# Optimization experiments

Hardware: AMD Instinct MI355X
Metric: run time of the kernel (lower is better)

Reference implementation:

```python
import jax, jax.numpy as jnp
import numpy as np

R_MAX = 5.0
AVG_NEIGH = 16.0
NUM_RADIAL = 8
F = 64            # channels per irrep (num_features)
S = 10            # num_species
LDIM = 16         # (max_ell+1)^2 for max_ell=3
L_SLICES = [(0, 1), (1, 4), (4, 9), (9, 16)]  # lm ranges for l=0..3
N_NODES = 10000
N_EDGES = 160000
HID_R = 64        # radial MLP hidden
HID_READ = 32     # readout MLP hidden


def sph_harm(v):
    # real spherical-harmonic polynomials up to l=3 (component convention fixed by this reference)
    x, y, z = v[:, 0], v[:, 1], v[:, 2]
    r2 = x * x + y * y + z * z
    return jnp.stack([
        jnp.ones_like(x),
        x, y, z,
        x * y, y * z, 3.0 * z * z - r2, x * z, x * x - y * y,
        y * (3.0 * x * x - y * y), x * y * z, y * (5.0 * z * z - r2),
        z * (5.0 * z * z - 3.0 * r2), x * (5.0 * z * z - r2),
        z * (x * x - y * y), x * (x * x - 3.0 * y * y),
    ], axis=-1)  # [E,16]


def radial_embedding(r):
    # Bessel basis with polynomial envelope (RadialEmbeddingBlock)
    u = r / R_MAX
    k = jnp.arange(1, NUM_RADIAL + 1, dtype=r.dtype)
    env = jnp.where(u < 1.0, (1.0 - u) ** 2 * (1.0 + 2.0 * u), 0.0)
    return jnp.sin(jnp.pi * k[None, :] * u[:, None]) / (u[:, None] + 1e-6) * env[:, None]


def species_linear(feats, W):
    # species-indexed e3nn Linear: per-l channel mixing. feats [N,F,16], W [N,4,F,F]
    outs = []
    for l, (a, b) in enumerate(L_SLICES):
        outs.append(jnp.einsum('nfm,nfg->ngm', feats[:, :, a:b], W[:, l]))
    return jnp.concatenate(outs, axis=-1)


def interaction(feats, Y, Remb, w1, w2, senders, receivers, n_nodes):
    # InteractionBlock: radial MLP -> tensor-product messages -> scatter-sum
    E = Y.shape[0]
    R = (jax.nn.silu(Remb @ w1) @ w2).reshape(E, F, 4, 2)  # per-l, per-path radial weights
    fs = feats[senders]            # [E,F,16] gather (irregular access)
    s0 = fs[:, :, 0:1]             # sender scalar channel
    parts = []
    for l, (a, b) in enumerate(L_SLICES):
        # path A: 0e (x) l -> l ;  path B: l (x) 0e -> l
        m_l = R[:, :, l, 0:1] * s0 * Y[:, None, a:b] + R[:, :, l, 1:2] * fs[:, :, a:b]
        parts.append(m_l)
    m = jnp.concatenate(parts, axis=-1)  # [E,F,16]
    agg = jax.ops.segment_sum(m, receivers, num_segments=n_nodes)
    return agg / jnp.sqrt(jnp.asarray(AVG_NEIGH, m.dtype))


def setup_inputs() -> dict:
    key = jax.random.key(0)
    ks = jax.random.split(key, 16)
    inp = {
        'vectors': jax.random.normal(ks[0], (N_EDGES, 3), jnp.float32) * 1.5,
        'node_specie': jax.random.randint(ks[1], (N_NODES,), 0, S, jnp.int32),
        'senders': jax.random.randint(ks[2], (N_EDGES,), 0, N_NODES, jnp.int32),
        'receivers': jax.random.randint(ks[3], (N_EDGES,), 0, N_NODES, jnp.int32),
        'w_embed': jax.random.normal(ks[4], (S, F), jnp.float32),
        'w_r1': jax.random.normal(ks[5], (2, NUM_RADIAL, HID_R), jnp.float32) / np.sqrt(NUM_RADIAL),
        'w_r2': jax.random.normal(ks[6], (2, HID_R, F * 4 * 2), jnp.float32) / np.sqrt(HID_R),
        'w_skip': jax.random.normal(ks[7], (2, S, 4, F, F), jnp.float32) / np.sqrt(F),
        'w_poly': jax.random.normal(ks[8], (2, 3, S, F), jnp.float32) * 0.1,
        'w_read0': jax.random.normal(ks[9], (F, 1), jnp.float32) / np.sqrt(F),
        'w_mlp1': jax.random.normal(ks[10], (F, HID_READ), jnp.float32) / np.sqrt(F),
        'w_mlp2': jax.random.normal(ks[11], (HID_READ, 1), jnp.float32) / np.sqrt(HID_READ),
    }
    return inp


def reference(vectors, node_specie, senders, receivers,
              w_embed, w_r1, w_r2, w_skip, w_poly,
              w_read0, w_mlp1, w_mlp2):
    N = node_specie.shape[0]
    senders = senders.astype(jnp.int32)
    receivers = receivers.astype(jnp.int32)
    r = jnp.sqrt(jnp.sum(vectors ** 2, axis=-1) + 1e-12)
    Y = sph_harm(vectors / r[:, None])
    Remb = radial_embedding(r)
    # node embedding -> scalar (l=0) channel only
    feats = jnp.zeros((N, F, LDIM), vectors.dtype).at[:, :, 0].set(w_embed[node_specie])
    outs = []
    for i in range(2):
        Wn = w_skip[i][node_specie]  # [N,4,F,F] species-indexed weights
        if i == 0:
            agg = interaction(feats, Y, Remb, w_r1[i], w_r2[i], senders, receivers, N)
            h = species_linear(agg, Wn)   # skip_tp_first
            sc = None
        else:
            sc = species_linear(feats, Wn)  # skip connection
            h = interaction(feats, Y, Remb, w_r1[i], w_r2[i], senders, receivers, N)
        # EquivariantProductBasisBlock (correlation=3): degree-3 invariant polynomial gate
        c = w_poly[i][:, node_specie]       # [3,N,F]
        s = h[:, :, 0]
        scale = c[0] + c[1] * s + c[2] * s * s
        feats = h * scale[:, :, None]
        if sc is not None:
            feats = feats + sc
        if i == 0:
            outs.append(feats[:, :, 0] @ w_read0)                       # LinearReadoutBlock
        else:
            outs.append(jax.nn.silu(feats[:, :, 0] @ w_mlp1) @ w_mlp2)  # NonLinearReadoutBlock
    return jnp.stack(outs, axis=1)  # [N, num_interactions, 1]
```

## Files before the change

### kernel.cpp

```cpp
#include <hip/hip_runtime.h>
#include <math.h>

#define F 64
#define LDIM 16
#define NRAD 8
#define HID_R 64
#define HID_READ 32
#define NSPEC 10

typedef __attribute__((ext_vector_type(8))) short short8v;
typedef __attribute__((ext_vector_type(4))) float f32x4;

__device__ __forceinline__ int l_of_m(int m) {
    return (m == 0) ? 0 : (m < 4) ? 1 : (m < 9) ? 2 : 3;
}
__device__ __forceinline__ float silu(float x) { return x / (1.0f + __expf(-x)); }
__device__ __forceinline__ unsigned short bf16bits(float x) {
    unsigned int u = __float_as_uint(x);
    u += 0x7fffu + ((u >> 16) & 1u);
    return (unsigned short)(u >> 16);
}
__device__ __forceinline__ float bf16tof(unsigned short b) {
    return __uint_as_float(((unsigned int)b) << 16);
}
__device__ __forceinline__ float lanebcast(float v, int l) {
    return __uint_as_float(__builtin_amdgcn_readlane(__float_as_uint(v), l));
}

__device__ __forceinline__ void geo_core(const float* __restrict__ vectors, int e,
                                         float* Ye_out, float* remb_out) {
    float vx = vectors[e * 3 + 0];
    float vy = vectors[e * 3 + 1];
    float vz = vectors[e * 3 + 2];
    float r = sqrtf(vx * vx + vy * vy + vz * vz + 1e-12f);
    float x = vx / r, y = vy / r, z = vz / r;
    float r2 = x * x + y * y + z * z;
    Ye_out[0]  = 1.0f;  Ye_out[1] = x;  Ye_out[2] = y;  Ye_out[3] = z;
    Ye_out[4]  = x * y; Ye_out[5] = y * z; Ye_out[6] = 3.0f * z * z - r2; Ye_out[7] = x * z;
    Ye_out[8]  = x * x - y * y;
    Ye_out[9]  = y * (3.0f * x * x - y * y);
    Ye_out[10] = x * y * z;
    Ye_out[11] = y * (5.0f * z * z - r2);
    Ye_out[12] = z * (5.0f * z * z - 3.0f * r2);
    Ye_out[13] = x * (5.0f * z * z - r2);
    Ye_out[14] = z * (x * x - y * y);
    Ye_out[15] = x * (x * x - 3.0f * y * y);
    float u = r / 5.0f;
    float env = (u < 1.0f) ? (1.0f - u) * (1.0f - u) * (1.0f + 2.0f * u) : 0.0f;
    float inv = env / (u + 1e-6f);
    const float PI = 3.14159265358979323846f;
#pragma unroll
    for (int k = 1; k <= NRAD; k++) remb_out[k - 1] = sinf(PI * (float)k * u) * inv;
}

__device__ __forceinline__ void hid_write(const float* remb, const float* w1,
                                          unsigned short* __restrict__ Hb, int e) {
    float h[HID_R];
#pragma unroll
    for (int j = 0; j < HID_R; j++) {
        float a = 0.0f;
#pragma unroll
        for (int k = 0; k < NRAD; k++) a += remb[k] * w1[k * HID_R + j];
        h[j] = silu(a);
    }
    unsigned int* dst = (unsigned int*)(Hb + (size_t)e * HID_R);
#pragma unroll
    for (int w = 0; w < 32; w++) {
        unsigned int lo = bf16bits(h[2 * w]);
        unsigned int hi = bf16bits(h[2 * w + 1]);
        dst[w] = lo | (hi << 16);
    }
}

__global__ void k1_kernel(const float* __restrict__ vectors,
                          const float* __restrict__ w_r1,
                          const float* __restrict__ w_r2,
                          const int* __restrict__ receivers,
                          float* __restrict__ Y,
                          unsigned short* __restrict__ Hb,
                          int* __restrict__ cnt,
                          unsigned short* __restrict__ w2f,
                          int E, int ngeo) {
    const int bid = blockIdx.x;
    if (bid >= ngeo) {
        const int layer = bid - ngeo;
        const float* src = w_r2 + (size_t)layer * HID_R * 512;
        unsigned short* dst = w2f + (size_t)layer * 32768;
        for (int idx = threadIdx.x; idx < 32768; idx += 256) {
            int j    = idx & 7;
            int lane = (idx >> 3) & 63;
            int ks   = (idx >> 9) & 1;
            int ct   = idx >> 10;
            int k    = ks * 32 + (lane >> 4) * 8 + j;
            int col  = ct * 16 + (lane & 15);
            dst[idx] = bf16bits(src[k * 512 + col]);
        }
        return;
    }
    const int e = bid * 256 + threadIdx.x;
    if (e >= E) return;
    atomicAdd(&cnt[receivers[e]], 1);
    float ye[16], remb[NRAD];
    geo_core(vectors, e, ye, remb);
    float4* Yd = (float4*)(Y + (size_t)e * 16);
    Yd[0] = make_float4(ye[0], ye[1], ye[2], ye[3]);
    Yd[1] = make_float4(ye[4], ye[5], ye[6], ye[7]);
    Yd[2] = make_float4(ye[8], ye[9], ye[10], ye[11]);
    Yd[3] = make_float4(ye[12], ye[13], ye[14], ye[15]);
    hid_write(remb, w_r1, Hb, e);
}

__global__ void geo_kernel(const float* __restrict__ vectors,
                           float* __restrict__ Y, float* __restrict__ Remb, int E) {
    int e = blockIdx.x * 256 + threadIdx.x;
    if (e >= E) return;
    float ye[16], remb[NRAD];
    geo_core(vectors, e, ye, remb);
#pragma unroll
    for (int m = 0; m < 16; m++) Y[(size_t)e * 16 + m] = ye[m];
#pragma unroll
    for (int k = 0; k < NRAD; k++) Remb[(size_t)e * NRAD + k] = remb[k];
}

__global__ void scan_kernel(const int* __restrict__ cnt, int* __restrict__ offs, int N) {
    __shared__ int buf[256];
    __shared__ int carry;
    int t = threadIdx.x;
    if (t == 0) carry = 0;
    __syncthreads();
    for (int base = 0; base < N; base += 256) {
        int v = (base + t < N) ? cnt[base + t] : 0;
        buf[t] = v;
        __syncthreads();
#pragma unroll
        for (int off = 1; off < 256; off <<= 1) {
            int x = (t >= off) ? buf[t - off] : 0;
            __syncthreads();
            buf[t] += x;
            __syncthreads();
        }
        if (base + t < N) offs[base + t] = carry + buf[t] - v;
        __syncthreads();
        if (t == 0) carry += buf[255];
        __syncthreads();
    }
    if (t == 0) offs[N] = carry;
}

__global__ void scatter_kernel(const int* __restrict__ receivers,
                               const int* __restrict__ senders,
                               const int* __restrict__ offs, int* __restrict__ cur,
                               int* __restrict__ eidx, int* __restrict__ snd_csr,
                               int* __restrict__ rcv_csr, int E) {
    int e = blockIdx.x * 256 + threadIdx.x;
    if (e >= E) return;
    int r = receivers[e];
    int pos = atomicAdd(&cur[r], 1);
    int t = offs[r] + pos;
    eidx[t] = e;
    snd_csr[t] = senders[e];
    rcv_csr[t] = r;
}

__global__ void init_feats_kernel(const float* __restrict__ w_embed,
                                  const int* __restrict__ specie,
                                  float* __restrict__ feats_t, int N) {
    int n = blockIdx.x;
    int sp = specie[n];
    for (int i = threadIdx.x; i < F * LDIM; i += 256) {
        int m = i >> 6;
        int f = i & 63;
        feats_t[(size_t)n * (F * LDIM) + i] = (m == 0) ? w_embed[sp * F + f] : 0.0f;
    }
}

template <bool L0>
__global__ __launch_bounds__(256, 4)
void fused_edge_kernel(const unsigned short* __restrict__ Hb,
                       const unsigned short* __restrict__ w2fl,
                       const float* __restrict__ Y,
                       const unsigned short* __restrict__ featsB,
                       const float* __restrict__ w_embed,
                       const int* __restrict__ specie,
                       const int* __restrict__ offs,
                       const int* __restrict__ eidx,
                       const int* __restrict__ snd_csr,
                       const int* __restrict__ rcv_csr,
                       float* __restrict__ agg, int N) {
    __shared__ float R_lds[16 * 532];
    __shared__ float ysL[16][16];
    __shared__ int   ssL[16];
    __shared__ int   rsL[16];
    const int tid = threadIdx.x;
    const int wave = tid >> 6, lane = tid & 63;
    const int lo = lane & 15, hi = lane >> 4;
    const int n0 = blockIdx.x * 2;
    const int segS = offs[n0], segE = offs[n0 + 2];
    const int mbase = wave * 4;

    int cur = -1;
    float acc[4] = {0.f, 0.f, 0.f, 0.f};

    for (int base = segS; base < segE; base += 16) {
        const int bend = (base + 16 < segE) ? base + 16 : segE;
        const int tcnt = bend - base;
        {
            const int t = tid >> 4, m = tid & 15;
            const int pos = base + t;
            const int cp = (pos < segE) ? pos : (segE - 1);
            ysL[t][m] = Y[(size_t)eidx[cp] * 16 + m];
            if (tid < 16) {
                const int p2 = base + tid;
                const int c2 = (p2 < segE) ? p2 : (segE - 1);
                const int s = snd_csr[c2];
                ssL[tid] = L0 ? specie[s] : s;
                rsL[tid] = rcv_csr[c2];
            }
        }
        {
            const int pos = base + lo;
            const int cp = (pos < segE) ? pos : (segE - 1);
            const int eid = eidx[cp];
            const unsigned short* hrow = Hb + (size_t)eid * 64;
            const short8v a0 = *(const short8v*)(hrow + hi * 8);
            const short8v a1 = *(const short8v*)(hrow + 32 + hi * 8);
            f32x4 c16[8];
#pragma unroll
            for (int i = 0; i < 8; i++) c16[i] = (f32x4)(0.f);
#pragma unroll
            for (int tt = 0; tt < 8; tt++) {
                const int ct = wave * 8 + tt;
                const short8v b0 = *(const short8v*)(w2fl + ct * 1024 + lane * 8);
                const short8v b1 = *(const short8v*)(w2fl + ct * 1024 + 512 + lane * 8);
                c16[tt] = __builtin_amdgcn_mfma_f32_16x16x32_bf16(a0, b0, c16[tt], 0, 0, 0);
                c16[tt] = __builtin_amdgcn_mfma_f32_16x16x32_bf16(a1, b1, c16[tt], 0, 0, 0);
            }
            const int lc = lo & 7;
#pragma unroll
            for (int tt = 0; tt < 8; tt++) {
                const int ct = wave * 8 + tt;
                const int f = ct * 2 + (lo >> 3);
#pragma unroll
                for (int r = 0; r < 4; r++) {
                    const int el = hi * 4 + r;
                    R_lds[el * 532 + lc * 66 + f] = c16[tt][r];
                }
            }
        }
        __syncthreads();
        {
            float ps0, pf[4] = {0.f, 0.f, 0.f, 0.f};
            if (L0) {
                ps0 = w_embed[ssL[0] * 64 + lane];
            } else {
                const unsigned short* f_ = featsB + (size_t)ssL[0] * 1024;
                ps0 = bf16tof(f_[lane]);
#pragma unroll
                for (int j = 0; j < 4; j++) pf[j] = bf16tof(f_[(mbase + j) * 64 + lane]);
            }
            for (int k = 0; k < tcnt; k++) {
                float ns0 = 0.f, nf[4] = {0.f, 0.f, 0.f, 0.f};
                const int kn = (k + 1 < tcnt) ? k + 1 : k;
                if (L0) {
                    ns0 = w_embed[ssL[kn] * 64 + lane];
                } else {
                    const unsigned short* f_ = featsB + (size_t)ssL[kn] * 1024;
                    ns0 = bf16tof(f_[lane]);
#pragma unroll
                    for (int j = 0; j < 4; j++) nf[j] = bf16tof(f_[(mbase + j) * 64 + lane]);
                }
                const int node = rsL[k];
                if (node != cur) {
                    if (cur >= 0) {
#pragma unroll
                        for (int j = 0; j < 4; j++)
                            agg[(size_t)cur * 1024 + (mbase + j) * 64 + lane] = acc[j] * 0.25f;
                    }
#pragma unroll
                    for (int j = 0; j < 4; j++) acc[j] = 0.f;
                    cur = node;
                }
                const float* Rt = R_lds + k * 532;
#pragma unroll
                for (int j = 0; j < 4; j++) {
                    const int m = mbase + j;
                    const int l = l_of_m(m);
                    const float r0 = Rt[(2 * l) * 66 + lane];
                    const float r1 = Rt[(2 * l + 1) * 66 + lane];
                    const float ym = ysL[k][m];
                    const float fsm = L0 ? ((m == 0) ? ps0 : 0.f) : pf[j];
                    acc[j] += r0 * ps0 * ym + r1 * fsm;
                }
                ps0 = ns0;
                if (!L0) {
#pragma unroll
                    for (int j = 0; j < 4; j++) pf[j] = nf[j];
                }
            }
        }
        __syncthreads();
    }
    if (cur >= 0) {
#pragma unroll
        for (int j = 0; j < 4; j++)
            agg[(size_t)cur * 1024 + (mbase + j) * 64 + lane] = acc[j] * 0.25f;
    }
#pragma unroll
    for (int d = 0; d < 2; d++) {
        const int nn = n0 + d;
        if (nn < N && offs[nn] == offs[nn + 1]) {
#pragma unroll
            for (int j = 0; j < 4; j++)
                agg[(size_t)nn * 1024 + (mbase + j) * 64 + lane] = 0.f;
        }
    }
}

__global__ void k2_kernel(const float* __restrict__ agg,
                          const int* __restrict__ specie,
                          const float* __restrict__ w_skip0,
                          const float* __restrict__ w_poly0,
                          const float* __restrict__ w_read0,
                          unsigned short* __restrict__ featsB,
                          float* __restrict__ featsF,
                          int useBF16,
                          float* __restrict__ out, int N,
                          const float* __restrict__ vectors,
                          const float* __restrict__ w1L1,
                          unsigned short* __restrict__ Hb, int E) {
    if (blockIdx.x >= N) {
        const int e = (blockIdx.x - N) * 256 + threadIdx.x;
        if (e >= E) return;
        float ye[16], remb[NRAD];
        geo_core(vectors, e, ye, remb);
        hid_write(remb, w1L1, Hb, e);
        return;
    }
    const int n = blockIdx.x;
    const int g = threadIdx.x & 63;
    const int mb = threadIdx.x >> 6;
    const int sp = specie[n];
    const float* W = w_skip0 + (size_t)sp * 4 * F * F;

    float areg[4];
#pragma unroll
    for (int j = 0; j < 4; j++) areg[j] = agg[(size_t)n * 1024 + (mb * 4 + j) * 64 + g];

    float h[4] = {0.f, 0.f, 0.f, 0.f};
    if (mb == 0) {
        const float* W0 = W;
        const float* W1 = W + 4096;
#pragma unroll
        for (int f = 0; f < 64; f++) {
            const float w0 = W0[f * 64 + g];
            const float w1 = W1[f * 64 + g];
            h[0] += lanebcast(areg[0], f) * w0;
            h[1] += lanebcast(areg[1], f) * w1;
            h[2] += lanebcast(areg[2], f) * w1;
            h[3] += lanebcast(areg[3], f) * w1;
        }
    } else if (mb == 1) {
        const float* W2 = W + 8192;
#pragma unroll
        for (int f = 0; f < 64; f++) {
            const float w2 = W2[f * 64 + g];
            h[0] += lanebcast(areg[0], f) * w2;
            h[1] += lanebcast(areg[1], f) * w2;
            h[2] += lanebcast(areg[2], f) * w2;
            h[3] += lanebcast(areg[3], f) * w2;
        }
    } else if (mb == 2) {
        const float* W2 = W + 8192;
        const float* W3 = W + 12288;
#pragma unroll
        for (int f = 0; f < 64; f++) {
            const float w2 = W2[f * 64 + g];
            const float w3 = W3[f * 64 + g];
            h[0] += lanebcast(areg[0], f) * w2;
            h[1] += lanebcast(areg[1], f) * w3;
            h[2] += lanebcast(areg[2], f) * w3;
            h[3] += lanebcast(areg[3], f) * w3;
        }
    } else {
        const float* W3 = W + 12288;
#pragma unroll
        for (int f = 0; f < 64; f++) {
            const float w3 = W3[f * 64 + g];
            h[0] += lanebcast(areg[0], f) * w3;
            h[1] += lanebcast(areg[1], f) * w3;
            h[2] += lanebcast(areg[2], f) * w3;
            h[3] += lanebcast(areg[3], f) * w3;
        }
    }

    __shared__ float h0L[64];
    if (mb == 0) h0L[g] = h[0];
    __syncthreads();
    const float s = h0L[g];
    const float c0 = w_poly0[(0 * NSPEC + sp) * F + g];
    const float c1 = w_poly0[(1 * NSPEC + sp) * F + g];
    const float c2 = w_poly0[(2 * NSPEC + sp) * F + g];
    const float scale = c0 + c1 * s + c2 * s * s;
    float f0val = 0.0f;
#pragma unroll
    for (int j = 0; j < 4; j++) {
        const int m = mb * 4 + j;
        const float fv = h[j] * scale;
        const size_t idx = (size_t)n * 1024 + m * 64 + g;
        if (useBF16) featsB[idx] = bf16bits(fv);
        else         featsF[idx] = fv;
        if (m == 0) f0val = fv;
    }
    if (mb == 0) {
        float v = f0val * w_read0[g];
#pragma unroll
        for (int off = 32; off > 0; off >>= 1) v += __shfl_down(v, off);
        if (g == 0) out[(size_t)n * 2 + 0] = v;
    }
}

__global__ void node1_kernel(const float* __restrict__ agg,
                             const unsigned short* __restrict__ featsB,
                             const int* __restrict__ specie,
                             const float* __restrict__ w_skip1,
                             const float* __restrict__ w_poly1,
                             const float* __restrict__ w_mlp1,
                             const float* __restrict__ w_mlp2,
                             float* __restrict__ out, int N) {
    const int wave = threadIdx.x >> 6;
    const int lane = threadIdx.x & 63;
    const int n = blockIdx.x * 4 + wave;
    const int sp = specie[n];
    const float* W0 = w_skip1 + (size_t)sp * 4 * F * F;
    const float fv = bf16tof(featsB[(size_t)n * 1024 + lane]);
    float sc0 = 0.0f;
#pragma unroll
    for (int f = 0; f < F; f++) {
        sc0 += lanebcast(fv, f) * W0[f * F + lane];
    }
    const float h0 = agg[(size_t)n * 1024 + lane];
    const float c0 = w_poly1[(0 * NSPEC + sp) * F + lane];
    const float c1 = w_poly1[(1 * NSPEC + sp) * F + lane];
    const float c2 = w_poly1[(2 * NSPEC + sp) * F + lane];
    const float scale = c0 + c1 * h0 + c2 * h0 * h0;
    const float f2 = h0 * scale + sc0;
    float acc = 0.0f;
#pragma unroll
    for (int gg = 0; gg < F; gg++) {
        const float fg = lanebcast(f2, gg);
        if (lane < HID_READ) acc += fg * w_mlp1[gg * HID_READ + lane];
    }
    float o = 0.0f;
    if (lane < HID_READ) o = silu(acc) * w_mlp2[lane];
#pragma unroll
    for (int off = 32; off > 0; off >>= 1) o += __shfl_down(o, off);
    if (lane == 0) out[(size_t)n * 2 + 1] = o;
}

__global__ void node1f_kernel(const float* __restrict__ agg,
                              const float* __restrict__ feats,
                              const int* __restrict__ specie,
                              const float* __restrict__ w_skip1,
                              const float* __restrict__ w_poly1,
                              const float* __restrict__ w_mlp1,
                              const float* __restrict__ w_mlp2,
                              float* __restrict__ out, int N) {
    const int wave = threadIdx.x >> 6;
    const int lane = threadIdx.x & 63;
    const int n = blockIdx.x * 4 + wave;
    const int sp = specie[n];
    const float* W0 = w_skip1 + (size_t)sp * 4 * F * F;
    const float fv = feats[(size_t)n * 1024 + lane];
    float sc0 = 0.0f;
#pragma unroll 8
    for (int f = 0; f < F; f++) {
        const float ff = __shfl(fv, f);
        sc0 += ff * W0[f * F + lane];
    }
    const float h0 = agg[(size_t)n * 1024 + lane];
    const float c0 = w_poly1[(0 * NSPEC + sp) * F + lane];
    const float c1 = w_poly1[(1 * NSPEC + sp) * F + lane];
    const float c2 = w_poly1[(2 * NSPEC + sp) * F + lane];
    const float scale = c0 + c1 * h0 + c2 * h0 * h0;
    const float f2 = h0 * scale + sc0;
    float acc = 0.0f;
#pragma unroll 8
    for (int gg = 0; gg < F; gg++) {
        const float fg = __shfl(f2, gg);
        if (lane < HID_READ) acc += fg * w_mlp1[gg * HID_READ + lane];
    }
    float o = 0.0f;
    if (lane < HID_READ) o = silu(acc) * w_mlp2[lane];
#pragma unroll
    for (int off = 32; off > 0; off >>= 1) o += __shfl_down(o, off);
    if (lane == 0) out[(size_t)n * 2 + 1] = o;
}

__global__ void edge_kernel(const float* __restrict__ Y, const float* __restrict__ Remb,
                            const float* __restrict__ feats_t,
                            const int* __restrict__ senders, const int* __restrict__ receivers,
                            const float* __restrict__ w1, const float* __restrict__ w2,
                            float* __restrict__ agg_t, int E) {
    const int wave = threadIdx.x >> 6;
    const int lane = threadIdx.x & 63;
    const int e = blockIdx.x * 4 + wave;
    __shared__ float hbuf[4][64];
    const float* remb = Remb + (size_t)e * NRAD;
    float acc = 0.0f;
#pragma unroll
    for (int k = 0; k < NRAD; k++) acc += remb[k] * w1[k * F + lane];
    hbuf[wave][lane] = silu(acc);
    __syncthreads();
    float r8[8] = {0.f, 0.f, 0.f, 0.f, 0.f, 0.f, 0.f, 0.f};
    const float* w2base = w2 + lane * 8;
#pragma unroll 8
    for (int j = 0; j < HID_R; j++) {
        float hj = hbuf[wave][j];
        const float4 a = *(const float4*)(w2base + j * 512);
        const float4 b = *(const float4*)(w2base + j * 512 + 4);
        r8[0] += hj * a.x; r8[1] += hj * a.y; r8[2] += hj * a.z; r8[3] += hj * a.w;
        r8[4] += hj * b.x; r8[5] += hj * b.y; r8[6] += hj * b.z; r8[7] += hj * b.w;
    }
    const int snd = senders[e];
    const int rcv = receivers[e];
    const float* fsrc = feats_t + (size_t)snd * (F * LDIM);
    float* adst = agg_t + (size_t)rcv * (F * LDIM);
    const float s0 = fsrc[lane];
    const float* Ye = Y + (size_t)e * 16;
#pragma unroll
    for (int m = 0; m < LDIM; m++) {
        const int l = l_of_m(m);
        const float ym = Ye[m];
        const float fsm = fsrc[m * F + lane];
        const float val = r8[l * 2 + 0] * s0 * ym + r8[l * 2 + 1] * fsm;
        atomicAdd(adst + m * F + lane, val * 0.25f);
    }
}

static inline size_t alignup(size_t x) { return (x + 255) & ~(size_t)255; }

extern "C" void kernel_launch(void* const* d_in, const int* in_sizes, int n_in,
                              void* d_out, int out_size, void* d_ws, size_t ws_size,
                              hipStream_t stream) {
    const float* vectors   = (const float*)d_in[0];
    const int*   specie    = (const int*)d_in[1];
    const int*   senders   = (const int*)d_in[2];
    const int*   receivers = (const int*)d_in[3];
    const float* w_embed   = (const float*)d_in[4];
    const float* w_r1      = (const float*)d_in[5];
    const float* w_r2      = (const float*)d_in[6];
    const float* w_skip    = (const float*)d_in[7];
    const float* w_poly    = (const float*)d_in[8];
    const float* w_read0   = (const float*)d_in[9];
    const float* w_mlp1    = (const float*)d_in[10];
    const float* w_mlp2    = (const float*)d_in[11];
    float* out = (float*)d_out;

    const int E = in_sizes[0] / 3;
    const int N = in_sizes[1];
    const int ngeo = (E + 255) / 256;

    char* base = (char*)d_ws;
    size_t off = 0;
    float* Y      = (float*)(base + off); off += alignup((size_t)E * 16 * sizeof(float));
    unsigned short* featsB = (unsigned short*)(base + off); off += alignup((size_t)N * F * LDIM * sizeof(unsigned short));
    float* agg    = (float*)(base + off); off += alignup((size_t)N * F * LDIM * sizeof(float));
    unsigned short* Hb = (unsigned short*)(base + off); off += alignup((size_t)E * 64 * sizeof(unsigned short));
    int* cnt      = (int*)(base + off);   off += alignup((size_t)N * sizeof(int));
    int* cur      = (int*)(base + off);   off += alignup((size_t)N * sizeof(int));
    int* offs     = (int*)(base + off);   off += alignup((size_t)(N + 1) * sizeof(int));
    int* eidx     = (int*)(base + off);   off += alignup((size_t)E * sizeof(int));
    int* snd_csr  = (int*)(base + off);   off += alignup((size_t)E * sizeof(int));
    int* rcv_csr  = (int*)(base + off);   off += alignup((size_t)E * sizeof(int));
    unsigned short* w2f = (unsigned short*)(base + off); off += alignup((size_t)2 * 32768 * sizeof(unsigned short));
    const size_t need = off;

    const size_t aggBytes = (size_t)N * F * LDIM * sizeof(float);

    if (ws_size >= need) {
        hipMemsetAsync(cnt, 0, (size_t)N * sizeof(int), stream);
        hipMemsetAsync(cur, 0, (size_t)N * sizeof(int), stream);
        k1_kernel<<<ngeo + 2, 256, 0, stream>>>(vectors, w_r1, w_r2, receivers,
                                                Y, Hb, cnt, w2f, E, ngeo);
        scan_kernel<<<1, 256, 0, stream>>>(cnt, offs, N);
        scatter_kernel<<<ngeo, 256, 0, stream>>>(receivers, senders, offs, cur,
                                                 eidx, snd_csr, rcv_csr, E);
        fused_edge_kernel<true><<<N / 2, 256, 0, stream>>>(
            Hb, w2f, Y, nullptr, w_embed, specie, offs, eidx, snd_csr, rcv_csr, agg, N);
        k2_kernel<<<N + ngeo, 256, 0, stream>>>(agg, specie,
                                                w_skip + (size_t)0 * NSPEC * 4 * F * F,
                                                w_poly + (size_t)0 * 3 * NSPEC * F,
                                                w_read0, featsB, nullptr, 1, out, N,
                                                vectors, w_r1 + NRAD * HID_R, Hb, E);
        fused_edge_kernel<false><<<N / 2, 256, 0, stream>>>(
            Hb, w2f + 32768, Y, featsB, w_embed, specie, offs, eidx, snd_csr, rcv_csr, agg, N);
        node1_kernel<<<N / 4, 256, 0, stream>>>(agg, featsB, specie,
                                                w_skip + (size_t)1 * NSPEC * 4 * F * F,
                                                w_poly + (size_t)1 * 3 * NSPEC * F,
                                                w_mlp1, w_mlp2, out, N);
    } else {
        size_t fo = 0;
        float* Yf    = (float*)(base + fo); fo += alignup((size_t)E * 16 * sizeof(float));
        float* Remb  = (float*)(base + fo); fo += alignup((size_t)E * NRAD * sizeof(float));
        float* featsF= (float*)(base + fo); fo += alignup((size_t)N * F * LDIM * sizeof(float));
        float* aggF  = (float*)(base + fo);

        geo_kernel<<<ngeo, 256, 0, stream>>>(vectors, Yf, Remb, E);
        init_feats_kernel<<<N, 256, 0, stream>>>(w_embed, specie, featsF, N);
        hipMemsetAsync(aggF, 0, aggBytes, stream);
        edge_kernel<<<E / 4, 256, 0, stream>>>(Yf, Remb, featsF, senders, receivers,
                                               w_r1, w_r2, aggF, E);
        k2_kernel<<<N, 256, 0, stream>>>(aggF, specie,
                                         w_skip + (size_t)0 * NSPEC * 4 * F * F,
                                         w_poly + (size_t)0 * 3 * NSPEC * F,
                                         w_read0, nullptr, featsF, 0, out, N,
                                         vectors, w_r1 + NRAD * HID_R, nullptr, 0);
        hipMemsetAsync(aggF, 0, aggBytes, stream);
        edge_kernel<<<E / 4, 256, 0, stream>>>(Yf, Remb, featsF, senders, receivers,
                                               w_r1 + NRAD * HID_R, w_r2 + HID_R * 512,
                                               aggF, E);
        node1f_kernel<<<N / 4, 256, 0, stream>>>(aggF, featsF, specie,
                                                 w_skip + (size_t)1 * NSPEC * 4 * F * F,
                                                 w_poly + (size_t)1 * 3 * NSPEC * F,
                                                 w_mlp1, w_mlp2, out, N);
    }
}
```

Measured before the change: 387.4 us.

## Assign one wave per receiver node with channel-major bf16 features and wider scan

The edge kernel now handles four receiver nodes per block, and each wave owns one node and accumulates all 16 lm components in registers. This replaces the old split where each wave held four components and tracked node changes through a receiver CSR array, so the rcv_csr array and its writes go away. The bf16 feature buffer is transposed so each lane reads its 16 components with two 16-byte vector loads, and the prefix scan uses 1024 threads. In exchange, three of the four waves sit idle while each 16-edge tile's per-node work runs, and register pressure rises with 16 accumulators.

```diff
diff --git a/kernel.cpp b/kernel.cpp
--- a/kernel.cpp
+++ b/kernel.cpp
@@ -123,17 +123,17 @@
 }
 
 __global__ void scan_kernel(const int* __restrict__ cnt, int* __restrict__ offs, int N) {
-    __shared__ int buf[256];
+    __shared__ int buf[1024];
     __shared__ int carry;
     int t = threadIdx.x;
     if (t == 0) carry = 0;
     __syncthreads();
-    for (int base = 0; base < N; base += 256) {
+    for (int base = 0; base < N; base += 1024) {
         int v = (base + t < N) ? cnt[base + t] : 0;
         buf[t] = v;
         __syncthreads();
 #pragma unroll
-        for (int off = 1; off < 256; off <<= 1) {
+        for (int off = 1; off < 1024; off <<= 1) {
             int x = (t >= off) ? buf[t - off] : 0;
             __syncthreads();
             buf[t] += x;
@@ -141,7 +141,7 @@
         }
         if (base + t < N) offs[base + t] = carry + buf[t] - v;
         __syncthreads();
-        if (t == 0) carry += buf[255];
+        if (t == 0) carry += buf[1023];
         __syncthreads();
     }
     if (t == 0) offs[N] = carry;
@@ -150,8 +150,7 @@
 __global__ void scatter_kernel(const int* __restrict__ receivers,
                                const int* __restrict__ senders,
                                const int* __restrict__ offs, int* __restrict__ cur,
-                               int* __restrict__ eidx, int* __restrict__ snd_csr,
-                               int* __restrict__ rcv_csr, int E) {
+                               int* __restrict__ eidx, int* __restrict__ snd_csr, int E) {
     int e = blockIdx.x * 256 + threadIdx.x;
     if (e >= E) return;
     int r = receivers[e];
@@ -159,7 +158,6 @@
     int t = offs[r] + pos;
     eidx[t] = e;
     snd_csr[t] = senders[e];
-    rcv_csr[t] = r;
 }
 
 __global__ void init_feats_kernel(const float* __restrict__ w_embed,
@@ -179,31 +177,33 @@
 void fused_edge_kernel(const unsigned short* __restrict__ Hb,
                        const unsigned short* __restrict__ w2fl,
                        const float* __restrict__ Y,
-                       const unsigned short* __restrict__ featsB,
+                       const unsigned short* __restrict__ featsBt,
                        const float* __restrict__ w_embed,
                        const int* __restrict__ specie,
                        const int* __restrict__ offs,
                        const int* __restrict__ eidx,
                        const int* __restrict__ snd_csr,
-                       const int* __restrict__ rcv_csr,
                        float* __restrict__ agg, int N) {
     __shared__ float R_lds[16 * 532];
     __shared__ float ysL[16][16];
     __shared__ int   ssL[16];
-    __shared__ int   rsL[16];
     const int tid = threadIdx.x;
     const int wave = tid >> 6, lane = tid & 63;
     const int lo = lane & 15, hi = lane >> 4;
-    const int n0 = blockIdx.x * 2;
-    const int segS = offs[n0], segE = offs[n0 + 2];
-    const int mbase = wave * 4;
-
-    int cur = -1;
-    float acc[4] = {0.f, 0.f, 0.f, 0.f};
+    const int n0 = blockIdx.x * 4;
+    const int n4 = (n0 + 4 < N) ? n0 + 4 : N;
+    const int segS = offs[n0], segE = offs[n4];
+    const int nw = n0 + wave;
+    const bool haveNode = (nw < N);
+    const int myS = haveNode ? offs[nw] : 0;
+    const int myE = haveNode ? offs[nw + 1] : 0;
+
+    float acc[16];
+#pragma unroll
+    for (int m = 0; m < 16; m++) acc[m] = 0.f;
 
     for (int base = segS; base < segE; base += 16) {
         const int bend = (base + 16 < segE) ? base + 16 : segE;
-        const int tcnt = bend - base;
         {
             const int t = tid >> 4, m = tid & 15;
             const int pos = base + t;
@@ -214,7 +214,6 @@
                 const int c2 = (p2 < segE) ? p2 : (segE - 1);
                 const int s = snd_csr[c2];
                 ssL[tid] = L0 ? specie[s] : s;
-                rsL[tid] = rcv_csr[c2];
             }
         }
         {
@@ -249,70 +248,71 @@
         }
         __syncthreads();
         {
-            float ps0, pf[4] = {0.f, 0.f, 0.f, 0.f};
-            if (L0) {
-                ps0 = w_embed[ssL[0] * 64 + lane];
-            } else {
-                const unsigned short* f_ = featsB + (size_t)ssL[0] * 1024;
-                ps0 = bf16tof(f_[lane]);
-#pragma unroll
-                for (int j = 0; j < 4; j++) pf[j] = bf16tof(f_[(mbase + j) * 64 + lane]);
-            }
-            for (int k = 0; k < tcnt; k++) {
-                float ns0 = 0.f, nf[4] = {0.f, 0.f, 0.f, 0.f};
-                const int kn = (k + 1 < tcnt) ? k + 1 : k;
+            const int a = (base > myS) ? base : myS;
+            const int b = (bend < myE) ? bend : myE;
+            if (a < b) {
+                float ps0 = 0.f;
+                unsigned pq[8];
                 if (L0) {
-                    ns0 = w_embed[ssL[kn] * 64 + lane];
+                    ps0 = w_embed[ssL[a - base] * 64 + lane];
                 } else {
-                    const unsigned short* f_ = featsB + (size_t)ssL[kn] * 1024;
-                    ns0 = bf16tof(f_[lane]);
-#pragma unroll
-                    for (int j = 0; j < 4; j++) nf[j] = bf16tof(f_[(mbase + j) * 64 + lane]);
+                    const unsigned short* fb = featsBt + (size_t)ssL[a - base] * 1024 + lane * 16;
+                    const uint4 q0 = *(const uint4*)fb;
+                    const uint4 q1 = *(const uint4*)(fb + 8);
+                    pq[0] = q0.x; pq[1] = q0.y; pq[2] = q0.z; pq[3] = q0.w;
+                    pq[4] = q1.x; pq[5] = q1.y; pq[6] = q1.z; pq[7] = q1.w;
+                    ps0 = __uint_as_float(pq[0] << 16);
                 }
-                const int node = rsL[k];
-                if (node != cur) {
-                    if (cur >= 0) {
-#pragma unroll
-                        for (int j = 0; j < 4; j++)
-                            agg[(size_t)cur * 1024 + (mbase + j) * 64 + lane] = acc[j] * 0.25f;
+                for (int pos = a; pos < b; ++pos) {
+                    const int k = pos - base;
+                    float ns0 = 0.f;
+                    unsigned nq[8];
+                    const int kn = (pos + 1 < b) ? (pos + 1 - base) : k;
+                    if (L0) {
+                        ns0 = w_embed[ssL[kn] * 64 + lane];
+                    } else {
+                        const unsigned short* fb = featsBt + (size_t)ssL[kn] * 1024 + lane * 16;
+                        const uint4 q0 = *(const uint4*)fb;
+                        const uint4 q1 = *(const uint4*)(fb + 8);
+                        nq[0] = q0.x; nq[1] = q0.y; nq[2] = q0.z; nq[3] = q0.w;
+                        nq[4] = q1.x; nq[5] = q1.y; nq[6] = q1.z; nq[7] = q1.w;
+                        ns0 = __uint_as_float(nq[0] << 16);
                     }
-#pragma unroll
-                    for (int j = 0; j < 4; j++) acc[j] = 0.f;
-                    cur = node;
-                }
-                const float* Rt = R_lds + k * 532;
-#pragma unroll
-                for (int j = 0; j < 4; j++) {
-                    const int m = mbase + j;
-                    const int l = l_of_m(m);
-                    const float r0 = Rt[(2 * l) * 66 + lane];
-                    const float r1 = Rt[(2 * l + 1) * 66 + lane];
-                    const float ym = ysL[k][m];
-                    const float fsm = L0 ? ((m == 0) ? ps0 : 0.f) : pf[j];
-                    acc[j] += r0 * ps0 * ym + r1 * fsm;
-                }
-                ps0 = ns0;
-                if (!L0) {
-#pragma unroll
-                    for (int j = 0; j < 4; j++) pf[j] = nf[j];
+                    const float* Rt = R_lds + k * 532;
+                    float r0[4], r1[4];
+#pragma unroll
+                    for (int l = 0; l < 4; l++) {
+                        r0[l] = Rt[(2 * l) * 66 + lane];
+                        r1[l] = Rt[(2 * l + 1) * 66 + lane];
+                    }
+#pragma unroll
+                    for (int m = 0; m < 16; m++) {
+                        const int l = l_of_m(m);
+                        const float ym = ysL[k][m];
+                        float fsm;
+                        if (L0) {
+                            fsm = (m == 0) ? ps0 : 0.f;
+                        } else {
+                            fsm = __uint_as_float((m & 1) ? (pq[m >> 1] & 0xffff0000u)
+                                                          : (pq[m >> 1] << 16));
+                        }
+                        acc[m] += r0[l] * ps0 * ym + r1[l] * fsm;
+                    }
+                    ps0 = ns0;
+                    if (!L0) {
+#pragma unroll
+                        for (int i = 0; i < 8; i++) pq[i] = nq[i];
+                    }
                 }
             }
         }
         __syncthreads();
     }
-    if (cur >= 0) {
-#pragma unroll
-        for (int j = 0; j < 4; j++)
-            agg[(size_t)cur * 1024 + (mbase + j) * 64 + lane] = acc[j] * 0.25f;
-    }
-#pragma unroll
-    for (int d = 0; d < 2; d++) {
-        const int nn = n0 + d;
-        if (nn < N && offs[nn] == offs[nn + 1]) {
-#pragma unroll
-            for (int j = 0; j < 4; j++)
-                agg[(size_t)nn * 1024 + (mbase + j) * 64 + lane] = 0.f;
-        }
+    if (haveNode) {
+        const float sc = (myS == myE) ? 0.f : 0.25f;
+#pragma unroll
+        for (int m = 0; m < 16; m++)
+            agg[(size_t)nw * 1024 + m * 64 + lane] = acc[m] * sc;
     }
 }
 
@@ -321,7 +321,7 @@
                           const float* __restrict__ w_skip0,
                           const float* __restrict__ w_poly0,
                           const float* __restrict__ w_read0,
-                          unsigned short* __restrict__ featsB,
+                          unsigned short* __restrict__ featsBt,
                           float* __restrict__ featsF,
                           int useBF16,
                           float* __restrict__ out, int N,
@@ -401,18 +401,22 @@
     const float c1 = w_poly0[(1 * NSPEC + sp) * F + g];
     const float c2 = w_poly0[(2 * NSPEC + sp) * F + g];
     const float scale = c0 + c1 * s + c2 * s * s;
-    float f0val = 0.0f;
-#pragma unroll
-    for (int j = 0; j < 4; j++) {
-        const int m = mb * 4 + j;
-        const float fv = h[j] * scale;
-        const size_t idx = (size_t)n * 1024 + m * 64 + g;
-        if (useBF16) featsB[idx] = bf16bits(fv);
-        else         featsF[idx] = fv;
-        if (m == 0) f0val = fv;
+    float fv[4];
+#pragma unroll
+    for (int j = 0; j < 4; j++) fv[j] = h[j] * scale;
+
+    if (useBF16) {
+        ushort4 pk;
+        pk.x = bf16bits(fv[0]); pk.y = bf16bits(fv[1]);
+        pk.z = bf16bits(fv[2]); pk.w = bf16bits(fv[3]);
+        *(ushort4*)(featsBt + (size_t)n * 1024 + g * 16 + mb * 4) = pk;
+    } else {
+#pragma unroll
+        for (int j = 0; j < 4; j++)
+            featsF[(size_t)n * 1024 + (mb * 4 + j) * 64 + g] = fv[j];
     }
     if (mb == 0) {
-        float v = f0val * w_read0[g];
+        float v = fv[0] * w_read0[g];
 #pragma unroll
         for (int off = 32; off > 0; off >>= 1) v += __shfl_down(v, off);
         if (g == 0) out[(size_t)n * 2 + 0] = v;
@@ -420,7 +424,7 @@
 }
 
 __global__ void node1_kernel(const float* __restrict__ agg,
-                             const unsigned short* __restrict__ featsB,
+                             const unsigned short* __restrict__ featsBt,
                              const int* __restrict__ specie,
                              const float* __restrict__ w_skip1,
                              const float* __restrict__ w_poly1,
@@ -432,7 +436,7 @@
     const int n = blockIdx.x * 4 + wave;
     const int sp = specie[n];
     const float* W0 = w_skip1 + (size_t)sp * 4 * F * F;
-    const float fv = bf16tof(featsB[(size_t)n * 1024 + lane]);
+    const float fv = bf16tof(featsBt[(size_t)n * 1024 + lane * 16]);
     float sc0 = 0.0f;
 #pragma unroll
     for (int f = 0; f < F; f++) {
@@ -563,7 +567,7 @@
     char* base = (char*)d_ws;
     size_t off = 0;
     float* Y      = (float*)(base + off); off += alignup((size_t)E * 16 * sizeof(float));
-    unsigned short* featsB = (unsigned short*)(base + off); off += alignup((size_t)N * F * LDIM * sizeof(unsigned short));
+    unsigned short* featsBt = (unsigned short*)(base + off); off += alignup((size_t)N * F * LDIM * sizeof(unsigned short));
     float* agg    = (float*)(base + off); off += alignup((size_t)N * F * LDIM * sizeof(float));
     unsigned short* Hb = (unsigned short*)(base + off); off += alignup((size_t)E * 64 * sizeof(unsigned short));
     int* cnt      = (int*)(base + off);   off += alignup((size_t)N * sizeof(int));
@@ -571,7 +575,6 @@
     int* offs     = (int*)(base + off);   off += alignup((size_t)(N + 1) * sizeof(int));
     int* eidx     = (int*)(base + off);   off += alignup((size_t)E * sizeof(int));
     int* snd_csr  = (int*)(base + off);   off += alignup((size_t)E * sizeof(int));
-    int* rcv_csr  = (int*)(base + off);   off += alignup((size_t)E * sizeof(int));
     unsigned short* w2f = (unsigned short*)(base + off); off += alignup((size_t)2 * 32768 * sizeof(unsigned short));
     const size_t need = off;
 
@@ -582,19 +585,19 @@
         hipMemsetAsync(cur, 0, (size_t)N * sizeof(int), stream);
         k1_kernel<<<ngeo + 2, 256, 0, stream>>>(vectors, w_r1, w_r2, receivers,
                                                 Y, Hb, cnt, w2f, E, ngeo);
-        scan_kernel<<<1, 256, 0, stream>>>(cnt, offs, N);
+        scan_kernel<<<1, 1024, 0, stream>>>(cnt, offs, N);
         scatter_kernel<<<ngeo, 256, 0, stream>>>(receivers, senders, offs, cur,
-                                                 eidx, snd_csr, rcv_csr, E);
-        fused_edge_kernel<true><<<N / 2, 256, 0, stream>>>(
-            Hb, w2f, Y, nullptr, w_embed, specie, offs, eidx, snd_csr, rcv_csr, agg, N);
+                                                 eidx, snd_csr, E);
+        fused_edge_kernel<true><<<(N + 3) / 4, 256, 0, stream>>>(
+            Hb, w2f, Y, nullptr, w_embed, specie, offs, eidx, snd_csr, agg, N);
         k2_kernel<<<N + ngeo, 256, 0, stream>>>(agg, specie,
                                                 w_skip + (size_t)0 * NSPEC * 4 * F * F,
                                                 w_poly + (size_t)0 * 3 * NSPEC * F,
-                                                w_read0, featsB, nullptr, 1, out, N,
+                                                w_read0, featsBt, nullptr, 1, out, N,
                                                 vectors, w_r1 + NRAD * HID_R, Hb, E);
-        fused_edge_kernel<false><<<N / 2, 256, 0, stream>>>(
-            Hb, w2f + 32768, Y, featsB, w_embed, specie, offs, eidx, snd_csr, rcv_csr, agg, N);
-        node1_kernel<<<N / 4, 256, 0, stream>>>(agg, featsB, specie,
+        fused_edge_kernel<false><<<(N + 3) / 4, 256, 0, stream>>>(
+            Hb, w2f + 32768, Y, featsBt, w_embed, specie, offs, eidx, snd_csr, agg, N);
+        node1_kernel<<<N / 4, 256, 0, stream>>>(agg, featsBt, specie,
                                                 w_skip + (size_t)1 * NSPEC * 4 * F * F,
                                                 w_poly + (size_t)1 * 3 * NSPEC * F,
                                                 w_mlp1, w_mlp2, out, N);
```

Result: no change. 392.0 us (+1.2%).

## Transpose bf16 node features to channel-major and pair radial weights in LDS

Applied to the files above, without the earlier changes.

Stores the bf16 intermediate features as [node][channel][m], so each lane fetches its four m-components for a sender with one 8-byte load instead of four strided 2-byte loads. The radial weights in LDS are interleaved as (path A, path B) pairs, so each edge step reads one float2 per l instead of two scalars, and the Y values are read as a float4. The prefix-scan kernel is widened from 256 to 1024 threads to cut the number of serial chunks. The bf16 writer in k2 and the reader in node1 are updated to the new layout, while the fp32 fallback path keeps the old layout.

```diff
diff --git a/kernel.cpp b/kernel.cpp
--- a/kernel.cpp
+++ b/kernel.cpp
@@ -123,17 +123,17 @@
 }
 
 __global__ void scan_kernel(const int* __restrict__ cnt, int* __restrict__ offs, int N) {
-    __shared__ int buf[256];
+    __shared__ int buf[1024];
     __shared__ int carry;
     int t = threadIdx.x;
     if (t == 0) carry = 0;
     __syncthreads();
-    for (int base = 0; base < N; base += 256) {
+    for (int base = 0; base < N; base += 1024) {
         int v = (base + t < N) ? cnt[base + t] : 0;
         buf[t] = v;
         __syncthreads();
 #pragma unroll
-        for (int off = 1; off < 256; off <<= 1) {
+        for (int off = 1; off < 1024; off <<= 1) {
             int x = (t >= off) ? buf[t - off] : 0;
             __syncthreads();
             buf[t] += x;
@@ -141,7 +141,7 @@
         }
         if (base + t < N) offs[base + t] = carry + buf[t] - v;
         __syncthreads();
-        if (t == 0) carry += buf[255];
+        if (t == 0) carry += buf[1023];
         __syncthreads();
     }
     if (t == 0) offs[N] = carry;
@@ -179,7 +179,7 @@
 void fused_edge_kernel(const unsigned short* __restrict__ Hb,
                        const unsigned short* __restrict__ w2fl,
                        const float* __restrict__ Y,
-                       const unsigned short* __restrict__ featsB,
+                       const unsigned short* __restrict__ featsBt,
                        const float* __restrict__ w_embed,
                        const int* __restrict__ specie,
                        const int* __restrict__ offs,
@@ -197,6 +197,8 @@
     const int n0 = blockIdx.x * 2;
     const int segS = offs[n0], segE = offs[n0 + 2];
     const int mbase = wave * 4;
+    const int lA = l_of_m(mbase);
+    const int lB = l_of_m(mbase + 1);
 
     int cur = -1;
     float acc[4] = {0.f, 0.f, 0.f, 0.f};
@@ -236,6 +238,8 @@
                 c16[tt] = __builtin_amdgcn_mfma_f32_16x16x32_bf16(a1, b1, c16[tt], 0, 0, 0);
             }
             const int lc = lo & 7;
+            const int pr = lc >> 1;
+            const int cc = lc & 1;
 #pragma unroll
             for (int tt = 0; tt < 8; tt++) {
                 const int ct = wave * 8 + tt;
@@ -243,31 +247,37 @@
 #pragma unroll
                 for (int r = 0; r < 4; r++) {
                     const int el = hi * 4 + r;
-                    R_lds[el * 532 + lc * 66 + f] = c16[tt][r];
+                    R_lds[el * 532 + pr * 132 + f * 2 + cc] = c16[tt][r];
                 }
             }
         }
         __syncthreads();
         {
-            float ps0, pf[4] = {0.f, 0.f, 0.f, 0.f};
-            if (L0) {
-                ps0 = w_embed[ssL[0] * 64 + lane];
-            } else {
-                const unsigned short* f_ = featsB + (size_t)ssL[0] * 1024;
-                ps0 = bf16tof(f_[lane]);
-#pragma unroll
-                for (int j = 0; j < 4; j++) pf[j] = bf16tof(f_[(mbase + j) * 64 + lane]);
+            float ps0 = 0.f;
+            unsigned pq0 = 0, pq1 = 0;
+            {
+                const int s = ssL[0];
+                if (L0) {
+                    ps0 = w_embed[s * 64 + lane];
+                } else {
+                    const unsigned short* fb = featsBt + (size_t)s * 1024 + lane * 16;
+                    const uint2 q = *(const uint2*)(fb + mbase);
+                    pq0 = q.x; pq1 = q.y;
+                    ps0 = bf16tof(fb[0]);
+                }
             }
             for (int k = 0; k < tcnt; k++) {
-                float ns0 = 0.f, nf[4] = {0.f, 0.f, 0.f, 0.f};
+                float ns0 = 0.f;
+                unsigned nq0 = 0, nq1 = 0;
                 const int kn = (k + 1 < tcnt) ? k + 1 : k;
+                const int sn = ssL[kn];
                 if (L0) {
-                    ns0 = w_embed[ssL[kn] * 64 + lane];
+                    ns0 = w_embed[sn * 64 + lane];
                 } else {
-                    const unsigned short* f_ = featsB + (size_t)ssL[kn] * 1024;
-                    ns0 = bf16tof(f_[lane]);
-#pragma unroll
-                    for (int j = 0; j < 4; j++) nf[j] = bf16tof(f_[(mbase + j) * 64 + lane]);
+                    const unsigned short* fb = featsBt + (size_t)sn * 1024 + lane * 16;
+                    const uint2 q = *(const uint2*)(fb + mbase);
+                    nq0 = q.x; nq1 = q.y;
+                    ns0 = bf16tof(fb[0]);
                 }
                 const int node = rsL[k];
                 if (node != cur) {
@@ -281,21 +291,20 @@
                     cur = node;
                 }
                 const float* Rt = R_lds + k * 532;
-#pragma unroll
-                for (int j = 0; j < 4; j++) {
-                    const int m = mbase + j;
-                    const int l = l_of_m(m);
-                    const float r0 = Rt[(2 * l) * 66 + lane];
-                    const float r1 = Rt[(2 * l + 1) * 66 + lane];
-                    const float ym = ysL[k][m];
-                    const float fsm = L0 ? ((m == 0) ? ps0 : 0.f) : pf[j];
-                    acc[j] += r0 * ps0 * ym + r1 * fsm;
-                }
+                const float2 pA = *(const float2*)(Rt + lA * 132 + lane * 2);
+                const float2 pB = *(const float2*)(Rt + lB * 132 + lane * 2);
+                const float4 ym4 = *(const float4*)&ysL[k][mbase];
+                const float fsm0 = L0 ? ((mbase == 0) ? ps0 : 0.f)
+                                      : __uint_as_float(pq0 << 16);
+                const float fsm1 = L0 ? 0.f : __uint_as_float(pq0 & 0xffff0000u);
+                const float fsm2 = L0 ? 0.f : __uint_as_float(pq1 << 16);
+                const float fsm3 = L0 ? 0.f : __uint_as_float(pq1 & 0xffff0000u);
+                acc[0] += pA.x * ps0 * ym4.x + pA.y * fsm0;
+                acc[1] += pB.x * ps0 * ym4.y + pB.y * fsm1;
+                acc[2] += pB.x * ps0 * ym4.z + pB.y * fsm2;
+                acc[3] += pB.x * ps0 * ym4.w + pB.y * fsm3;
                 ps0 = ns0;
-                if (!L0) {
-#pragma unroll
-                    for (int j = 0; j < 4; j++) pf[j] = nf[j];
-                }
+                pq0 = nq0; pq1 = nq1;
             }
         }
         __syncthreads();
@@ -321,7 +330,7 @@
                           const float* __restrict__ w_skip0,
                           const float* __restrict__ w_poly0,
                           const float* __restrict__ w_read0,
-                          unsigned short* __restrict__ featsB,
+                          unsigned short* __restrict__ featsBt,
                           float* __restrict__ featsF,
                           int useBF16,
                           float* __restrict__ out, int N,
@@ -401,18 +410,22 @@
     const float c1 = w_poly0[(1 * NSPEC + sp) * F + g];
     const float c2 = w_poly0[(2 * NSPEC + sp) * F + g];
     const float scale = c0 + c1 * s + c2 * s * s;
-    float f0val = 0.0f;
-#pragma unroll
-    for (int j = 0; j < 4; j++) {
-        const int m = mb * 4 + j;
-        const float fv = h[j] * scale;
-        const size_t idx = (size_t)n * 1024 + m * 64 + g;
-        if (useBF16) featsB[idx] = bf16bits(fv);
-        else         featsF[idx] = fv;
-        if (m == 0) f0val = fv;
+    float fv[4];
+#pragma unroll
+    for (int j = 0; j < 4; j++) fv[j] = h[j] * scale;
+
+    if (useBF16) {
+        ushort4 pk;
+        pk.x = bf16bits(fv[0]); pk.y = bf16bits(fv[1]);
+        pk.z = bf16bits(fv[2]); pk.w = bf16bits(fv[3]);
+        *(ushort4*)(featsBt + (size_t)n * 1024 + g * 16 + mb * 4) = pk;
+    } else {
+#pragma unroll
+        for (int j = 0; j < 4; j++)
+            featsF[(size_t)n * 1024 + (mb * 4 + j) * 64 + g] = fv[j];
     }
     if (mb == 0) {
-        float v = f0val * w_read0[g];
+        float v = fv[0] * w_read0[g];
 #pragma unroll
         for (int off = 32; off > 0; off >>= 1) v += __shfl_down(v, off);
         if (g == 0) out[(size_t)n * 2 + 0] = v;
@@ -420,7 +433,7 @@
 }
 
 __global__ void node1_kernel(const float* __restrict__ agg,
-                             const unsigned short* __restrict__ featsB,
+                             const unsigned short* __restrict__ featsBt,
                              const int* __restrict__ specie,
                              const float* __restrict__ w_skip1,
                              const float* __restrict__ w_poly1,
@@ -432,7 +445,7 @@
     const int n = blockIdx.x * 4 + wave;
     const int sp = specie[n];
     const float* W0 = w_skip1 + (size_t)sp * 4 * F * F;
-    const float fv = bf16tof(featsB[(size_t)n * 1024 + lane]);
+    const float fv = bf16tof(featsBt[(size_t)n * 1024 + lane * 16]);
     float sc0 = 0.0f;
 #pragma unroll
     for (int f = 0; f < F; f++) {
@@ -563,7 +576,7 @@
     char* base = (char*)d_ws;
     size_t off = 0;
     float* Y      = (float*)(base + off); off += alignup((size_t)E * 16 * sizeof(float));
-    unsigned short* featsB = (unsigned short*)(base + off); off += alignup((size_t)N * F * LDIM * sizeof(unsigned short));
+    unsigned short* featsBt = (unsigned short*)(base + off); off += alignup((size_t)N * F * LDIM * sizeof(unsigned short));
     float* agg    = (float*)(base + off); off += alignup((size_t)N * F * LDIM * sizeof(float));
     unsigned short* Hb = (unsigned short*)(base + off); off += alignup((size_t)E * 64 * sizeof(unsigned short));
     int* cnt      = (int*)(base + off);   off += alignup((size_t)N * sizeof(int));
@@ -582,7 +595,7 @@
         hipMemsetAsync(cur, 0, (size_t)N * sizeof(int), stream);
         k1_kernel<<<ngeo + 2, 256, 0, stream>>>(vectors, w_r1, w_r2, receivers,
                                                 Y, Hb, cnt, w2f, E, ngeo);
-        scan_kernel<<<1, 256, 0, stream>>>(cnt, offs, N);
+        scan_kernel<<<1, 1024, 0, stream>>>(cnt, offs, N);
         scatter_kernel<<<ngeo, 256, 0, stream>>>(receivers, senders, offs, cur,
                                                  eidx, snd_csr, rcv_csr, E);
         fused_edge_kernel<true><<<N / 2, 256, 0, stream>>>(
@@ -590,11 +603,11 @@
         k2_kernel<<<N + ngeo, 256, 0, stream>>>(agg, specie,
                                                 w_skip + (size_t)0 * NSPEC * 4 * F * F,
                                                 w_poly + (size_t)0 * 3 * NSPEC * F,
-                                                w_read0, featsB, nullptr, 1, out, N,
+                                                w_read0, featsBt, nullptr, 1, out, N,
                                                 vectors, w_r1 + NRAD * HID_R, Hb, E);
         fused_edge_kernel<false><<<N / 2, 256, 0, stream>>>(
-            Hb, w2f + 32768, Y, featsB, w_embed, specie, offs, eidx, snd_csr, rcv_csr, agg, N);
-        node1_kernel<<<N / 4, 256, 0, stream>>>(agg, featsB, specie,
+            Hb, w2f + 32768, Y, featsBt, w_embed, specie, offs, eidx, snd_csr, rcv_csr, agg, N);
+        node1_kernel<<<N / 4, 256, 0, stream>>>(agg, featsBt, specie,
                                                 w_skip + (size_t)1 * NSPEC * 4 * F * F,
                                                 w_poly + (size_t)1 * 3 * NSPEC * F,
                                                 w_mlp1, w_mlp2, out, N);
```

After: 374.9 us. 3.2% less time.
